# Performance work log

Measured on AMD Instinct MI355X. Metric: run time of the kernel, lower is better.

The kernel has to match this reference:

```python
import jax, jax.numpy as jnp
import numpy as np

B, KEY, D, U, MODES = 16384, 64, 128, 128, 32

def setup_inputs() -> dict:
    key = jax.random.key(0)
    k1, k2, k3, k4, k5 = jax.random.split(key, 5)
    return {
        "key": jax.random.normal(k1, (B, KEY), dtype=jnp.float32),
        "x": jax.random.normal(k2, (B, D), dtype=jnp.float32),
        "sens": jnp.ones((MODES,), dtype=jnp.float32),
        "keys_map": jax.random.normal(k3, (MODES, KEY), dtype=jnp.float32),
        "kernels": jax.random.normal(k4, (MODES, D, U), dtype=jnp.float32) * 0.05,
        "biases": jax.random.normal(k5, (MODES, U), dtype=jnp.float32) * 0.05,
    }

def reference(key, x, sens, keys_map, kernels, biases):
    # key: [B, KEY]; keys_map: [MODES, KEY]
    # Euclidean distance of each key to each mode's stored key.
    dist = jnp.sqrt(jnp.sum((key[:, None, :] - keys_map[None, :, :]) ** 2, axis=-1))  # [B, MODES]
    sim = jax.nn.softmax(sens / (dist + 1.0), axis=-1)  # [B, MODES]
    modes = kernels.shape[0]
    # Original: kernel_b = mean_m(sim[b,m] * kernels[m]); out_b = x_b @ kernel_b.
    # Reordered as GEMM-per-mode + weighted combine (same math):
    out = jnp.einsum('bm,bd,mdu->bu', sim, x, kernels) / modes  # [B, U]
    out = out + (sim @ biases) / modes  # mean over modes of sim-weighted biases
    return out
```

## Files before the change

### kernel.cpp

```cpp
#include <hip/hip_runtime.h>

#define BATCH 16384
#define KEYD  64
#define DDIM  128
#define UDIM  128
#define MODES 32

typedef __attribute__((ext_vector_type(8))) short bf16x8;
typedef __attribute__((ext_vector_type(4))) float f32x4;

__device__ __forceinline__ unsigned short f2bf(float f) {
  unsigned u = __float_as_uint(f);
  unsigned r = (u + 0x7FFFu + ((u >> 16) & 1u)) >> 16;
  return (unsigned short)r;
}

__device__ __forceinline__ void gld_lds16(const void* g, void* l) {
  __builtin_amdgcn_global_load_lds(
      (const __attribute__((address_space(1))) unsigned int*)g,
      (__attribute__((address_space(3))) unsigned int*)l, 16, 0, 0);
}

__global__ __launch_bounds__(256) void prep_all(
    const float* __restrict__ key, const float* __restrict__ x,
    const float* __restrict__ sens, const float* __restrict__ keys_map,
    const float* __restrict__ kernels, const float* __restrict__ biases,
    float* __restrict__ sim, unsigned short* __restrict__ x16,
    unsigned short* __restrict__ kb16, unsigned short* __restrict__ bb16) {
  const int t = threadIdx.x;
  const int bid = blockIdx.x;

  if (bid < BATCH / 32) {
    __shared__ float kr[32][KEYD];
    *(float4*)(&kr[0][0] + t * 4) =
        *(const float4*)(key + (long)bid * 32 * KEYD + t * 4);
    *(float4*)(&kr[0][0] + 1024 + t * 4) =
        *(const float4*)(key + (long)bid * 32 * KEYD + 1024 + t * 4);

    const int lane = t & 63, wave = t >> 6;
    const int m = lane & 31, h = lane >> 5;
    float kreg[32];
    {
      const float* kmp = keys_map + m * KEYD + h * 32;
      #pragma unroll
      for (int j = 0; j < 32; j += 4) {
        const float4 v = *(const float4*)(kmp + j);
        kreg[j] = v.x; kreg[j + 1] = v.y; kreg[j + 2] = v.z; kreg[j + 3] = v.w;
      }
    }
    const float sv = sens[m];
    __syncthreads();

    #pragma unroll
    for (int rr = 0; rr < 8; ++rr) {
      const int rl = wave * 8 + rr;
      const long row = (long)bid * 32 + rl;

      float d2h = 0.f;
      #pragma unroll
      for (int j = 0; j < 32; j += 2) {
        const float2 kv = *(const float2*)(&kr[rl][h * 32 + j]);
        float a = kv.x - kreg[j], b = kv.y - kreg[j + 1];
        d2h += a * a + b * b;
      }
      float d2 = d2h + __shfl_xor(d2h, 32, 64);
      float logit = sv / (sqrtf(d2) + 1.0f);
      float mx = logit;
      #pragma unroll
      for (int off = 16; off > 0; off >>= 1) mx = fmaxf(mx, __shfl_xor(mx, off, 64));
      float e = __expf(logit - mx);
      float s = e;
      #pragma unroll
      for (int off = 16; off > 0; off >>= 1) s += __shfl_xor(s, off, 64);
      if (h == 0) sim[row * MODES + m] = e / s;

      const float2 xv = *(const float2*)(x + row * DDIM + lane * 2);
      ushort2 o; o.x = f2bf(xv.x); o.y = f2bf(xv.y);
      *(ushort2*)(x16 + row * DDIM + lane * 2) = o;
    }
  } else {
    int tt = (bid - BATCH / 32) * 256 + t;
    if (tt < MODES * 16 * UDIM) {
      int u = tt & 127, kb = (tt >> 7) & 15, m = tt >> 11;
      const float* src = kernels + (long)((m * 16 + kb) * 8) * UDIM + u;
      ushort4 lo, hi;
      lo.x = f2bf(src[0 * UDIM]); lo.y = f2bf(src[1 * UDIM]);
      lo.z = f2bf(src[2 * UDIM]); lo.w = f2bf(src[3 * UDIM]);
      hi.x = f2bf(src[4 * UDIM]); hi.y = f2bf(src[5 * UDIM]);
      hi.z = f2bf(src[6 * UDIM]); hi.w = f2bf(src[7 * UDIM]);
      *(ushort4*)(kb16 + (long)tt * 8) = lo;
      *(ushort4*)(kb16 + (long)tt * 8 + 4) = hi;
    } else {
      int tb = tt - MODES * 16 * UDIM;
      int u = tb & 127, kb = tb >> 7;
      const float* src = biases + kb * 8 * UDIM + u;
      ushort4 lo, hi;
      lo.x = f2bf(src[0 * UDIM]); lo.y = f2bf(src[1 * UDIM]);
      lo.z = f2bf(src[2 * UDIM]); lo.w = f2bf(src[3 * UDIM]);
      hi.x = f2bf(src[4 * UDIM]); hi.y = f2bf(src[5 * UDIM]);
      hi.z = f2bf(src[6 * UDIM]); hi.w = f2bf(src[7 * UDIM]);
      *(ushort4*)(bb16 + (long)tb * 8) = lo;
      *(ushort4*)(bb16 + (long)tb * 8 + 4) = hi;
    }
  }
}

__global__ __launch_bounds__(256, 3) void gemm_poly(
    const unsigned short* __restrict__ x16, const unsigned short* __restrict__ kb16,
    const unsigned short* __restrict__ bb16, const float* __restrict__ sim,
    float* __restrict__ partial) {
  __shared__ alignas(16) unsigned short bsh[16 * 64 * 8];
  __shared__ alignas(16) float simT[8][128];

  const int t = threadIdx.x;
  const int lane = t & 63, w = t >> 6;
  const int q = lane >> 4, l16 = lane & 15;
  const int wrow = w * 32;
  const long bm = (long)blockIdx.x * 128;
  const int split = blockIdx.y & 3;
  const int c0 = (blockIdx.y >> 2) * 64;

  {
    int rrow = t >> 1, mg = (t & 1) * 4;
    const float4 v = *(const float4*)(sim + (bm + rrow) * MODES + split * 8 + mg);
    simT[mg + 0][rrow] = v.x; simT[mg + 1][rrow] = v.y;
    simT[mg + 2][rrow] = v.z; simT[mg + 3][rrow] = v.w;
  }

  bf16x8 aF[2][4];
  #pragma unroll
  for (int rt = 0; rt < 2; ++rt)
    #pragma unroll
    for (int ks = 0; ks < 4; ++ks)
      aF[rt][ks] = *(const bf16x8*)(x16 + (bm + wrow + rt * 16 + l16) * DDIM + ks * 32 + q * 8);

  f32x4 acc[2][4] = {};

  for (int mi = 0; mi < 8; ++mi) {
    const int m = split * 8 + mi;
    __syncthreads();
    {
      const unsigned short* msrc = kb16 + (long)m * (16 * UDIM * 8) + c0 * 8;
      #pragma unroll
      for (int i = 0; i < 4; ++i) {
        int e = (t + i * 256) * 8;
        int kblk = e >> 9, within = e & 511;
        gld_lds16(msrc + (long)kblk * (UDIM * 8) + within,
                  (unsigned short*)bsh + e);
      }
    }
    __syncthreads();

    bf16x8 bF[4][4];
    #pragma unroll
    for (int ks = 0; ks < 4; ++ks)
      #pragma unroll
      for (int ct = 0; ct < 4; ++ct)
        bF[ks][ct] = *(const bf16x8*)&bsh[(((ks * 4 + q) * 64) + ct * 16 + l16) * 8];

    #pragma unroll
    for (int rt = 0; rt < 2; ++rt) {
      f32x4 tmp[4] = {};
      #pragma unroll
      for (int ks = 0; ks < 4; ++ks)
        #pragma unroll
        for (int ct = 0; ct < 4; ++ct)
          tmp[ct] = __builtin_amdgcn_mfma_f32_16x16x32_bf16(aF[rt][ks], bF[ks][ct], tmp[ct], 0, 0, 0);
      const f32x4 s = *(const f32x4*)&simT[mi][wrow + rt * 16 + q * 4];
      #pragma unroll
      for (int ct = 0; ct < 4; ++ct)
        acc[rt][ct] += s * tmp[ct];
    }
  }

  if (split == 0) {
    bf16x8 sF[2];
    #pragma unroll
    for (int rt = 0; rt < 2; ++rt) {
      const float* sp = sim + (bm + wrow + rt * 16 + l16) * MODES + q * 8;
      bf16x8 f;
      #pragma unroll
      for (int j = 0; j < 8; ++j) f[j] = (short)f2bf(sp[j]);
      sF[rt] = f;
    }
    #pragma unroll
    for (int ct = 0; ct < 4; ++ct) {
      bf16x8 bb = *(const bf16x8*)(bb16 + (long)(q * UDIM + c0 + ct * 16 + l16) * 8);
      #pragma unroll
      for (int rt = 0; rt < 2; ++rt)
        acc[rt][ct] = __builtin_amdgcn_mfma_f32_16x16x32_bf16(sF[rt], bb, acc[rt][ct], 0, 0, 0);
    }
  }

  float* part = partial + (long)split * ((long)BATCH * UDIM);
  #pragma unroll
  for (int rt = 0; rt < 2; ++rt)
    #pragma unroll
    for (int ct = 0; ct < 4; ++ct) {
      long row = bm + wrow + rt * 16 + q * 4;
      int col = c0 + ct * 16 + l16;
      #pragma unroll
      for (int r = 0; r < 4; ++r)
        part[(row + r) * UDIM + col] = acc[rt][ct][r];
    }
}

__global__ __launch_bounds__(256) void reduce_parts(
    const float* __restrict__ partial, float* __restrict__ out) {
  const long i = ((long)blockIdx.x * 256 + threadIdx.x) * 4;
  const long S = (long)BATCH * UDIM;
  const f32x4 p0 = *(const f32x4*)(partial + i);
  const f32x4 p1 = *(const f32x4*)(partial + S + i);
  const f32x4 p2 = *(const f32x4*)(partial + 2 * S + i);
  const f32x4 p3 = *(const f32x4*)(partial + 3 * S + i);
  *(f32x4*)(out + i) = (p0 + p1 + p2 + p3) * (1.0f / MODES);
}

extern "C" void kernel_launch(void* const* d_in, const int* in_sizes, int n_in,
                              void* d_out, int out_size, void* d_ws, size_t ws_size,
                              hipStream_t stream) {
  const float* key      = (const float*)d_in[0];
  const float* x        = (const float*)d_in[1];
  const float* sens     = (const float*)d_in[2];
  const float* keys_map = (const float*)d_in[3];
  const float* kernels  = (const float*)d_in[4];
  const float* biases   = (const float*)d_in[5];
  float* out = (float*)d_out;

  char* ws = (char*)d_ws;
  float*          sim  = (float*)ws;
  unsigned short* x16  = (unsigned short*)(ws + (2u << 20));
  unsigned short* kb16 = (unsigned short*)(ws + (6u << 20));
  unsigned short* bb16 = (unsigned short*)(ws + (7u << 20));
  float*          part = (float*)(ws + (8u << 20));

  prep_all<<<BATCH / 32 + 258, 256, 0, stream>>>(
      key, x, sens, keys_map, kernels, biases, sim, x16, kb16, bb16);
  gemm_poly<<<dim3(BATCH / 128, 8), 256, 0, stream>>>(x16, kb16, bb16, sim, part);
  reduce_parts<<<(BATCH * UDIM) / (256 * 4), 256, 0, stream>>>(part, out);
}
```

Measured before the change: 110.4 us.

## Drop mode split-K and reduce kernel, double-buffer per-mode weight tiles in LDS

The GEMM kernel now loops over all 32 modes in each block instead of splitting the modes four ways. It writes the scaled output directly, which removes the partial-sum buffer traffic and the separate reduction launch. Per-mode weight tiles are double-buffered in LDS, so the next mode's global-to-LDS load overlaps the MFMA work on the current one. The trade-off is a grid four times smaller (256 blocks of 4 waves), which leaves less parallelism to hide latency, plus more LDS per block.

```diff
diff --git a/kernel.cpp b/kernel.cpp
--- a/kernel.cpp
+++ b/kernel.cpp
@@ -105,26 +105,29 @@
   }
 }
 
-__global__ __launch_bounds__(256, 3) void gemm_poly(
+__global__ __launch_bounds__(256) void gemm_poly(
     const unsigned short* __restrict__ x16, const unsigned short* __restrict__ kb16,
     const unsigned short* __restrict__ bb16, const float* __restrict__ sim,
-    float* __restrict__ partial) {
-  __shared__ alignas(16) unsigned short bsh[16 * 64 * 8];
-  __shared__ alignas(16) float simT[8][128];
+    float* __restrict__ out) {
+  __shared__ alignas(16) unsigned short bsh[2][16 * 64 * 8];
+  __shared__ alignas(16) float simT[MODES][128];
 
   const int t = threadIdx.x;
   const int lane = t & 63, w = t >> 6;
   const int q = lane >> 4, l16 = lane & 15;
   const int wrow = w * 32;
   const long bm = (long)blockIdx.x * 128;
-  const int split = blockIdx.y & 3;
-  const int c0 = (blockIdx.y >> 2) * 64;
+  const int c0 = blockIdx.y * 64;
 
   {
-    int rrow = t >> 1, mg = (t & 1) * 4;
-    const float4 v = *(const float4*)(sim + (bm + rrow) * MODES + split * 8 + mg);
-    simT[mg + 0][rrow] = v.x; simT[mg + 1][rrow] = v.y;
-    simT[mg + 2][rrow] = v.z; simT[mg + 3][rrow] = v.w;
+    int rrow = t >> 1, mg = (t & 1) * 16;
+    const float* sp = sim + (bm + rrow) * MODES + mg;
+    #pragma unroll
+    for (int g = 0; g < 4; ++g) {
+      const float4 v = *(const float4*)(sp + g * 4);
+      simT[mg + g * 4 + 0][rrow] = v.x; simT[mg + g * 4 + 1][rrow] = v.y;
+      simT[mg + g * 4 + 2][rrow] = v.z; simT[mg + g * 4 + 3][rrow] = v.w;
+    }
   }
 
   bf16x8 aF[2][4];
@@ -134,29 +137,36 @@
     for (int ks = 0; ks < 4; ++ks)
       aF[rt][ks] = *(const bf16x8*)(x16 + (bm + wrow + rt * 16 + l16) * DDIM + ks * 32 + q * 8);
 
+  #pragma unroll
+  for (int i = 0; i < 4; ++i) {
+    int e = (t + i * 256) * 8;
+    int kblk = e >> 9, within = e & 511;
+    gld_lds16(kb16 + c0 * 8 + (long)kblk * (UDIM * 8) + within,
+              (unsigned short*)&bsh[0][0] + e);
+  }
+
   f32x4 acc[2][4] = {};
 
-  for (int mi = 0; mi < 8; ++mi) {
-    const int m = split * 8 + mi;
+  for (int m = 0; m < MODES; ++m) {
     __syncthreads();
-    {
-      const unsigned short* msrc = kb16 + (long)m * (16 * UDIM * 8) + c0 * 8;
+    if (m < MODES - 1) {
+      const unsigned short* msrc = kb16 + (long)(m + 1) * (16 * UDIM * 8) + c0 * 8;
+      unsigned short* dst = &bsh[(m + 1) & 1][0];
       #pragma unroll
       for (int i = 0; i < 4; ++i) {
         int e = (t + i * 256) * 8;
         int kblk = e >> 9, within = e & 511;
-        gld_lds16(msrc + (long)kblk * (UDIM * 8) + within,
-                  (unsigned short*)bsh + e);
+        gld_lds16(msrc + (long)kblk * (UDIM * 8) + within, dst + e);
       }
     }
-    __syncthreads();
-
+
+    const unsigned short* bs = &bsh[m & 1][0];
     bf16x8 bF[4][4];
     #pragma unroll
     for (int ks = 0; ks < 4; ++ks)
       #pragma unroll
       for (int ct = 0; ct < 4; ++ct)
-        bF[ks][ct] = *(const bf16x8*)&bsh[(((ks * 4 + q) * 64) + ct * 16 + l16) * 8];
+        bF[ks][ct] = *(const bf16x8*)&bs[(((ks * 4 + q) * 64) + ct * 16 + l16) * 8];
 
     #pragma unroll
     for (int rt = 0; rt < 2; ++rt) {
@@ -166,14 +176,14 @@
         #pragma unroll
         for (int ct = 0; ct < 4; ++ct)
           tmp[ct] = __builtin_amdgcn_mfma_f32_16x16x32_bf16(aF[rt][ks], bF[ks][ct], tmp[ct], 0, 0, 0);
-      const f32x4 s = *(const f32x4*)&simT[mi][wrow + rt * 16 + q * 4];
+      const f32x4 s = *(const f32x4*)&simT[m][wrow + rt * 16 + q * 4];
       #pragma unroll
       for (int ct = 0; ct < 4; ++ct)
         acc[rt][ct] += s * tmp[ct];
     }
   }
 
-  if (split == 0) {
+  {
     bf16x8 sF[2];
     #pragma unroll
     for (int rt = 0; rt < 2; ++rt) {
@@ -192,7 +202,6 @@
     }
   }
 
-  float* part = partial + (long)split * ((long)BATCH * UDIM);
   #pragma unroll
   for (int rt = 0; rt < 2; ++rt)
     #pragma unroll
@@ -201,19 +210,8 @@
       int col = c0 + ct * 16 + l16;
       #pragma unroll
       for (int r = 0; r < 4; ++r)
-        part[(row + r) * UDIM + col] = acc[rt][ct][r];
-    }
-}
-
-__global__ __launch_bounds__(256) void reduce_parts(
-    const float* __restrict__ partial, float* __restrict__ out) {
-  const long i = ((long)blockIdx.x * 256 + threadIdx.x) * 4;
-  const long S = (long)BATCH * UDIM;
-  const f32x4 p0 = *(const f32x4*)(partial + i);
-  const f32x4 p1 = *(const f32x4*)(partial + S + i);
-  const f32x4 p2 = *(const f32x4*)(partial + 2 * S + i);
-  const f32x4 p3 = *(const f32x4*)(partial + 3 * S + i);
-  *(f32x4*)(out + i) = (p0 + p1 + p2 + p3) * (1.0f / MODES);
+        out[(row + r) * UDIM + col] = acc[rt][ct][r] * (1.0f / MODES);
+    }
 }
 
 extern "C" void kernel_launch(void* const* d_in, const int* in_sizes, int n_in,
@@ -232,10 +230,8 @@
   unsigned short* x16  = (unsigned short*)(ws + (2u << 20));
   unsigned short* kb16 = (unsigned short*)(ws + (6u << 20));
   unsigned short* bb16 = (unsigned short*)(ws + (7u << 20));
-  float*          part = (float*)(ws + (8u << 20));
 
   prep_all<<<BATCH / 32 + 258, 256, 0, stream>>>(
       key, x, sens, keys_map, kernels, biases, sim, x16, kb16, bb16);
-  gemm_poly<<<dim3(BATCH / 128, 8), 256, 0, stream>>>(x16, kb16, bb16, sim, part);
-  reduce_parts<<<(BATCH * UDIM) / (256 * 4), 256, 0, stream>>>(part, out);
-}
+  gemm_poly<<<dim3(BATCH / 128, 2), 256, 0, stream>>>(x16, kb16, bb16, sim, out);
+}
```

New measurement: 111.2 us. No clear change (+0.8%).

## Double-buffer kernel tiles in LDS and prefetch the next half-mode stage

Applied to the files above, without the earlier changes.

The GEMM loop now splits each mode's 128-deep K range into two 64-deep stages and keeps two LDS buffers. The global-to-LDS load for the next stage is issued before the MFMAs on the current one, so each iteration needs one barrier instead of two and the load latency overlaps compute. The catch is that the register fragment aF is now picked by a runtime stage index. If the 16-step loop is not fully unrolled, that could push aF to scratch memory. Correctness also depends on the async LDS loads being complete by the next barrier.

```diff
diff --git a/kernel.cpp b/kernel.cpp
--- a/kernel.cpp
+++ b/kernel.cpp
@@ -109,7 +109,7 @@
     const unsigned short* __restrict__ x16, const unsigned short* __restrict__ kb16,
     const unsigned short* __restrict__ bb16, const float* __restrict__ sim,
     float* __restrict__ partial) {
-  __shared__ alignas(16) unsigned short bsh[16 * 64 * 8];
+  __shared__ alignas(16) unsigned short bsh[2][8 * 64 * 8];
   __shared__ alignas(16) float simT[8][128];
 
   const int t = threadIdx.x;
@@ -134,38 +134,53 @@
     for (int ks = 0; ks < 4; ++ks)
       aF[rt][ks] = *(const bf16x8*)(x16 + (bm + wrow + rt * 16 + l16) * DDIM + ks * 32 + q * 8);
 
+  const unsigned short* kbase = kb16 + (long)(split * 8) * (16 * UDIM * 8);
+
+  {
+    #pragma unroll
+    for (int i = 0; i < 2; ++i) {
+      int e = (t + i * 256) * 8;
+      int kk = e >> 9, within = e & 511;
+      gld_lds16(kbase + ((long)kk * UDIM + c0) * 8 + within,
+                (unsigned short*)&bsh[0][0] + e);
+    }
+  }
+
   f32x4 acc[2][4] = {};
 
-  for (int mi = 0; mi < 8; ++mi) {
-    const int m = split * 8 + mi;
+  for (int S = 0; S < 16; ++S) {
+    const int mi = S >> 1, st = S & 1;
     __syncthreads();
-    {
-      const unsigned short* msrc = kb16 + (long)m * (16 * UDIM * 8) + c0 * 8;
-      #pragma unroll
-      for (int i = 0; i < 4; ++i) {
+    if (S < 15) {
+      const int mi2 = (S + 1) >> 1, st2 = (S + 1) & 1;
+      const unsigned short* src =
+          kbase + (long)mi2 * (16 * UDIM * 8) + ((long)st2 * 8 * UDIM + c0) * 8;
+      unsigned short* dst = &bsh[(S + 1) & 1][0];
+      #pragma unroll
+      for (int i = 0; i < 2; ++i) {
         int e = (t + i * 256) * 8;
-        int kblk = e >> 9, within = e & 511;
-        gld_lds16(msrc + (long)kblk * (UDIM * 8) + within,
-                  (unsigned short*)bsh + e);
+        int kk = e >> 9, within = e & 511;
+        gld_lds16(src + ((long)kk * UDIM) * 8 + within, dst + e);
       }
     }
-    __syncthreads();
-
-    bf16x8 bF[4][4];
-    #pragma unroll
-    for (int ks = 0; ks < 4; ++ks)
+
+    const unsigned short* bs = &bsh[S & 1][0];
+    bf16x8 bF[2][4];
+    #pragma unroll
+    for (int ksl = 0; ksl < 2; ++ksl)
       #pragma unroll
       for (int ct = 0; ct < 4; ++ct)
-        bF[ks][ct] = *(const bf16x8*)&bsh[(((ks * 4 + q) * 64) + ct * 16 + l16) * 8];
+        bF[ksl][ct] = *(const bf16x8*)&bs[(((ksl * 4 + q) * 64) + ct * 16 + l16) * 8];
 
     #pragma unroll
     for (int rt = 0; rt < 2; ++rt) {
       f32x4 tmp[4] = {};
       #pragma unroll
-      for (int ks = 0; ks < 4; ++ks)
+      for (int ksl = 0; ksl < 2; ++ksl)
         #pragma unroll
         for (int ct = 0; ct < 4; ++ct)
-          tmp[ct] = __builtin_amdgcn_mfma_f32_16x16x32_bf16(aF[rt][ks], bF[ks][ct], tmp[ct], 0, 0, 0);
+          tmp[ct] = __builtin_amdgcn_mfma_f32_16x16x32_bf16(
+              aF[rt][st * 2 + ksl], bF[ksl][ct], tmp[ct], 0, 0, 0);
       const f32x4 s = *(const f32x4*)&simT[mi][wrow + rt * 16 + q * 4];
       #pragma unroll
       for (int ct = 0; ct < 4; ++ct)
```

New measurement: 111.5 us. Within noise of the previous version (+1.0%).
